# Kernel tuning notes

Measured on AMD Instinct MI355X. Metric: run time of the kernel, lower is better.

## Reference

```python
import jax, jax.numpy as jnp
import numpy as np

LENGTHSCALE = 0.3
EPS = 1e-10
N = 100000   # evaluation points
M = 3375     # grid_size**3 RBF centers


def setup_inputs() -> dict:
    key = jax.random.key(0)
    k1, k2, k3, k4, k5 = jax.random.split(key, 5)
    x = jax.random.normal(k1, (N, 3), dtype=jnp.float32)
    centers = jax.random.normal(k2, (M, 3), dtype=jnp.float32)
    coeff_u = jax.random.normal(k3, (M,), dtype=jnp.float32)
    coeff_v = jax.random.normal(k4, (M,), dtype=jnp.float32)
    coeff_w = jax.random.normal(k5, (M,), dtype=jnp.float32)
    return {"x": x, "centers": centers, "coeff_u": coeff_u,
            "coeff_v": coeff_v, "coeff_w": coeff_w}


def reference(x, centers, coeff_u, coeff_v, coeff_w):
    # base sphere-attractor field: x * (1 - ||x||)
    r = jnp.linalg.norm(x, axis=-1, keepdims=True)          # (N, 1)
    base = x * (1.0 - r)                                    # (N, 3)

    x_sq = jnp.sum(x * x, axis=-1, keepdims=True)           # (N, 1)
    c_sq = jnp.sum(centers * centers, axis=-1)[None, :]     # (1, M)
    xy = x @ centers.T                                      # (N, M)
    dist2 = jnp.maximum(x_sq + c_sq - 2.0 * xy, EPS)        # (N, M)

    # RBF features and three shared-phi matvecs fused as one matmul
    phi = jnp.exp(-dist2 / (2.0 * LENGTHSCALE ** 2))        # (N, M)
    coeffs = jnp.stack([coeff_u, coeff_v, coeff_w], axis=1) # (M, 3)
    uvw = phi @ coeffs                                      # (N, 3)
    return base + uvw
```

## Files before the change

kernel.cpp:

```cpp
#include <hip/hip_runtime.h>
#include <hip/hip_bf16.h>

#define S2 8.014973f
#define K2 16.029946f
#define CHUNKS 8

typedef float f2 __attribute__((ext_vector_type(2)));

__global__ void rbf_prep_kernel(const float* __restrict__ centers,
                                const float* __restrict__ cu,
                                const float* __restrict__ cv,
                                const float* __restrict__ cw,
                                float4* __restrict__ cpack, int M) {
    int m = blockIdx.x * 256 + threadIdx.x;
    if (m < M) {
        float cx = centers[3 * m + 0];
        float cy = centers[3 * m + 1];
        float cz = centers[3 * m + 2];
        float4 a, b;
        a.x = K2 * cx;
        a.y = K2 * cy;
        a.z = K2 * cz;
        a.w = -S2 * (cx * cx + cy * cy + cz * cz);
        b.x = cu[m];
        b.y = cv[m];
        b.z = cw[m];
        b.w = 0.f;
        cpack[2 * m + 0] = a;
        cpack[2 * m + 1] = b;
    }
}

__global__ __launch_bounds__(512) void rbf_main_kernel(
    const float* __restrict__ x, const float4* __restrict__ cpack,
    float* __restrict__ out, int N, int M) {
    __shared__ float acc[CHUNKS][128][3];

    const int tid = threadIdx.x;
    const int lane = tid & 63;
    const int chunk = __builtin_amdgcn_readfirstlane(tid >> 6);
    const int pbase = blockIdx.x * 128;
    const int p0 = pbase + lane;
    const int p1 = pbase + 64 + lane;

    float x00 = 0.f, x01 = 0.f, x02 = 0.f;
    float x10 = 0.f, x11 = 0.f, x12 = 0.f;
    if (p0 < N) {
        x00 = x[3 * p0 + 0];
        x01 = x[3 * p0 + 1];
        x02 = x[3 * p0 + 2];
    }
    if (p1 < N) {
        x10 = x[3 * p1 + 0];
        x11 = x[3 * p1 + 1];
        x12 = x[3 * p1 + 2];
    }

    const f2 X = {x00, x10};
    const f2 Y = {x01, x11};
    const f2 Z = {x02, x12};
    const f2 PX = {-S2 * (x00 * x00 + x01 * x01 + x02 * x02),
                   -S2 * (x10 * x10 + x11 * x11 + x12 * x12)};

    const int per = (M + CHUNKS - 1) / CHUNKS;
    const int jb = chunk * per;
    const int je = min(jb + per, M);

    f2 au = {0.f, 0.f}, av = {0.f, 0.f}, aw = {0.f, 0.f};

#pragma unroll 4
    for (int j = jb; j < je; ++j) {
        const float4 a = cpack[2 * j + 0];
        const float4 b = cpack[2 * j + 1];
        f2 e = PX + a.w;
        e += Z * a.z;
        e += Y * a.y;
        e += X * a.x;
        f2 phi;
        phi.x = __builtin_amdgcn_exp2f(e.x);
        phi.y = __builtin_amdgcn_exp2f(e.y);
        au += phi * b.x;
        av += phi * b.y;
        aw += phi * b.z;
    }

    if (chunk == 0) {
        float g0 = 1.f - sqrtf(x00 * x00 + x01 * x01 + x02 * x02);
        au.x += x00 * g0;
        av.x += x01 * g0;
        aw.x += x02 * g0;
        float g1 = 1.f - sqrtf(x10 * x10 + x11 * x11 + x12 * x12);
        au.y += x10 * g1;
        av.y += x11 * g1;
        aw.y += x12 * g1;
    }

    acc[chunk][lane][0] = au.x;
    acc[chunk][lane][1] = av.x;
    acc[chunk][lane][2] = aw.x;
    acc[chunk][64 + lane][0] = au.y;
    acc[chunk][64 + lane][1] = av.y;
    acc[chunk][64 + lane][2] = aw.y;
    __syncthreads();

    const int out_n = 3 * N;
    if (tid < 384) {
        int gi = pbase * 3 + tid;
        if (gi < out_n) {
            int pl = tid / 3;
            int c = tid % 3;
            float s = 0.f;
#pragma unroll
            for (int k = 0; k < CHUNKS; ++k) s += acc[k][pl][c];
            out[gi] = s;
        }
    }
}

extern "C" void kernel_launch(void* const* d_in, const int* in_sizes, int n_in,
                              void* d_out, int out_size, void* d_ws,
                              size_t ws_size, hipStream_t stream) {
    const float* x = (const float*)d_in[0];
    const float* centers = (const float*)d_in[1];
    const float* cu = (const float*)d_in[2];
    const float* cv = (const float*)d_in[3];
    const float* cw = (const float*)d_in[4];
    const int N = in_sizes[0] / 3;
    const int M = in_sizes[1] / 3;
    float4* cpack = (float4*)d_ws;
    float* out = (float*)d_out;

    hipLaunchKernelGGL(rbf_prep_kernel, dim3((M + 255) / 256), dim3(256), 0,
                       stream, centers, cu, cv, cw, cpack, M);
    hipLaunchKernelGGL(rbf_main_kernel, dim3((N + 127) / 128), dim3(512), 0,
                       stream, x, cpack, out, N, M);
}
```

Baseline: 139.4 us.

## Split center range across blocks and combine partial sums with atomic adds

The main kernel now divides the RBF centers into CSPLIT=4 groups spread over separate blocks, so the grid is four times larger. Each block reduces its eight waves in shared memory and atomically adds the partial result into an output that is zeroed first with hipMemsetAsync. The aim is better CU load balance and less tail imbalance from having only ~782 large blocks. In exchange, x is loaded redundantly, there is an extra memset, and the atomics make the floating-point summation order nondeterministic. The loop unroll also goes from 4 to 8, and the memset size assumes out_size is in bytes, which may not hold.

```diff
diff --git a/kernel.cpp b/kernel.cpp
--- a/kernel.cpp
+++ b/kernel.cpp
@@ -1,9 +1,9 @@
 #include <hip/hip_runtime.h>
-#include <hip/hip_bf16.h>
 
 #define S2 8.014973f
 #define K2 16.029946f
-#define CHUNKS 8
+#define WAVES 8
+#define CSPLIT 4
 
 typedef float f2 __attribute__((ext_vector_type(2)));
 
@@ -34,12 +34,13 @@
 __global__ __launch_bounds__(512) void rbf_main_kernel(
     const float* __restrict__ x, const float4* __restrict__ cpack,
     float* __restrict__ out, int N, int M) {
-    __shared__ float acc[CHUNKS][128][3];
+    __shared__ float acc[WAVES][128][3];
 
     const int tid = threadIdx.x;
     const int lane = tid & 63;
-    const int chunk = __builtin_amdgcn_readfirstlane(tid >> 6);
-    const int pbase = blockIdx.x * 128;
+    const int wave = __builtin_amdgcn_readfirstlane(tid >> 6);
+    const int cs = blockIdx.x & (CSPLIT - 1);
+    const int pbase = (blockIdx.x / CSPLIT) * 128;
     const int p0 = pbase + lane;
     const int p1 = pbase + 64 + lane;
 
@@ -62,13 +63,15 @@
     const f2 PX = {-S2 * (x00 * x00 + x01 * x01 + x02 * x02),
                    -S2 * (x10 * x10 + x11 * x11 + x12 * x12)};
 
-    const int per = (M + CHUNKS - 1) / CHUNKS;
-    const int jb = chunk * per;
-    const int je = min(jb + per, M);
+    const int g = cs * WAVES + wave;
+    const int per = (M + WAVES * CSPLIT - 1) / (WAVES * CSPLIT);
+    const int jb = g * per;
+    int je = jb + per;
+    if (je > M) je = M;
 
     f2 au = {0.f, 0.f}, av = {0.f, 0.f}, aw = {0.f, 0.f};
 
-#pragma unroll 4
+#pragma unroll 8
     for (int j = jb; j < je; ++j) {
         const float4 a = cpack[2 * j + 0];
         const float4 b = cpack[2 * j + 1];
@@ -84,7 +87,7 @@
         aw += phi * b.z;
     }
 
-    if (chunk == 0) {
+    if (g == 0) {
         float g0 = 1.f - sqrtf(x00 * x00 + x01 * x01 + x02 * x02);
         au.x += x00 * g0;
         av.x += x01 * g0;
@@ -95,24 +98,22 @@
         aw.y += x12 * g1;
     }
 
-    acc[chunk][lane][0] = au.x;
-    acc[chunk][lane][1] = av.x;
-    acc[chunk][lane][2] = aw.x;
-    acc[chunk][64 + lane][0] = au.y;
-    acc[chunk][64 + lane][1] = av.y;
-    acc[chunk][64 + lane][2] = aw.y;
+    acc[wave][lane][0] = au.x;
+    acc[wave][lane][1] = av.x;
+    acc[wave][lane][2] = aw.x;
+    acc[wave][64 + lane][0] = au.y;
+    acc[wave][64 + lane][1] = av.y;
+    acc[wave][64 + lane][2] = aw.y;
     __syncthreads();
 
-    const int out_n = 3 * N;
     if (tid < 384) {
-        int gi = pbase * 3 + tid;
-        if (gi < out_n) {
-            int pl = tid / 3;
-            int c = tid % 3;
+        const int gi = pbase * 3 + tid;
+        if (gi < 3 * N) {
+            const float* af = &acc[0][0][0];
             float s = 0.f;
 #pragma unroll
-            for (int k = 0; k < CHUNKS; ++k) s += acc[k][pl][c];
-            out[gi] = s;
+            for (int k = 0; k < WAVES; ++k) s += af[k * 384 + tid];
+            unsafeAtomicAdd(&out[gi], s);
         }
     }
 }
@@ -132,6 +133,8 @@
 
     hipLaunchKernelGGL(rbf_prep_kernel, dim3((M + 255) / 256), dim3(256), 0,
                        stream, centers, cu, cv, cw, cpack, M);
-    hipLaunchKernelGGL(rbf_main_kernel, dim3((N + 127) / 128), dim3(512), 0,
+    hipMemsetAsync(d_out, 0, (size_t)out_size, stream);
+    const int pt = (N + 127) / 128;
+    hipLaunchKernelGGL(rbf_main_kernel, dim3(pt * CSPLIT), dim3(512), 0,
                        stream, x, cpack, out, N, M);
 }
```

Measured after the change: 126.5 us. -9.3%, faster.

## Compute RBF exponents with bf16 MFMA using hi/lo split precision

Applied to the files above, without the earlier changes.

Replaces the scalar FMA computation of the RBF exponent with a 16x16x32 bf16 MFMA. Center and point coordinates are split into hi/lo bf16 pairs so that the dot products plus the squared-norm terms come out near fp32 accuracy. Each 64-thread block handles 16 points against all centers, and the per-lane partial sums are combined with cross-lane shuffles instead of a shared-memory reduction. The aim is to take the exponent arithmetic off the VALU and leave mainly exp2 and the coefficient FMAs there. The risks are precision loss from the bf16 splitting, since the dropped lo*lo terms are scaled by the large exponent factor, and many small single-wave blocks.

```diff
diff --git a/kernel.cpp b/kernel.cpp
--- a/kernel.cpp
+++ b/kernel.cpp
@@ -1,119 +1,128 @@
 #include <hip/hip_runtime.h>
-#include <hip/hip_bf16.h>
 
 #define S2 8.014973f
 #define K2 16.029946f
-#define CHUNKS 8
+#define ONEB ((unsigned short)0x3F80)
 
-typedef float f2 __attribute__((ext_vector_type(2)));
+typedef float f32x4 __attribute__((ext_vector_type(4)));
+typedef short bf16x8 __attribute__((ext_vector_type(8)));
 
-__global__ void rbf_prep_kernel(const float* __restrict__ centers,
-                                const float* __restrict__ cu,
-                                const float* __restrict__ cv,
-                                const float* __restrict__ cw,
-                                float4* __restrict__ cpack, int M) {
-    int m = blockIdx.x * 256 + threadIdx.x;
-    if (m < M) {
-        float cx = centers[3 * m + 0];
-        float cy = centers[3 * m + 1];
-        float cz = centers[3 * m + 2];
-        float4 a, b;
-        a.x = K2 * cx;
-        a.y = K2 * cy;
-        a.z = K2 * cz;
-        a.w = -S2 * (cx * cx + cy * cy + cz * cz);
-        b.x = cu[m];
-        b.y = cv[m];
-        b.z = cw[m];
-        b.w = 0.f;
-        cpack[2 * m + 0] = a;
-        cpack[2 * m + 1] = b;
+__device__ __forceinline__ unsigned short bhi(float v) {
+    unsigned int b = __builtin_bit_cast(unsigned int, v);
+    return (unsigned short)((b + 0x7FFFu + ((b >> 16) & 1u)) >> 16);
+}
+__device__ __forceinline__ float bf2f(unsigned short h) {
+    unsigned int u = ((unsigned int)h) << 16;
+    return __builtin_bit_cast(float, u);
+}
+
+__global__ void rbf_prep(const float* __restrict__ centers,
+                         const float* __restrict__ cu,
+                         const float* __restrict__ cv,
+                         const float* __restrict__ cw,
+                         uint4* __restrict__ afrag,
+                         float* __restrict__ bpack, int M) {
+    const int T = blockIdx.x;
+    const int lane = threadIdx.x;
+    const int row = lane & 15, g = lane >> 4;
+    const int c = T * 16 + row;
+    float cx = 0.f, cy = 0.f, cz = 0.f;
+    if (c < M) { cx = centers[3*c]; cy = centers[3*c+1]; cz = centers[3*c+2]; }
+    const float a1 = K2 * cx, a2 = K2 * cy, a3 = K2 * cz;
+    const float a4 = -S2 * (cx*cx + cy*cy + cz*cz);
+    const unsigned short a1h = bhi(a1), a2h = bhi(a2), a3h = bhi(a3), a4h = bhi(a4);
+    const unsigned short a1l = bhi(a1 - bf2f(a1h));
+    const unsigned short a2l = bhi(a2 - bf2f(a2h));
+    const unsigned short a3l = bhi(a3 - bf2f(a3h));
+    const unsigned short a4l = bhi(a4 - bf2f(a4h));
+    const unsigned short F[16] = {a1h, a1h, a1l, a2h, a2h, a2l, a3h, a3h,
+                                  a3l, a4h, a4l, ONEB, ONEB, 0, 0, 0};
+    uint4 u;
+    u.x = (unsigned int)F[8*g+0] | ((unsigned int)F[8*g+1] << 16);
+    u.y = (unsigned int)F[8*g+2] | ((unsigned int)F[8*g+3] << 16);
+    u.z = (unsigned int)F[8*g+4] | ((unsigned int)F[8*g+5] << 16);
+    u.w = (unsigned int)F[8*g+6] | ((unsigned int)F[8*g+7] << 16);
+    afrag[T * 64 + lane] = u;
+
+    if (lane < 48) {
+        const int g2 = lane / 12, idx = lane % 12;
+        const int comp = idx >> 2, r = idx & 3;
+        const int c2 = T * 16 + g2 * 4 + r;
+        float v = 0.f;
+        if (c2 < M)
+            v = (comp == 0) ? cu[c2] : ((comp == 1) ? cv[c2] : cw[c2]);
+        bpack[(T * 12 + g2 * 3 + comp) * 4 + r] = v;
     }
 }
 
-__global__ __launch_bounds__(512) void rbf_main_kernel(
-    const float* __restrict__ x, const float4* __restrict__ cpack,
-    float* __restrict__ out, int N, int M) {
-    __shared__ float acc[CHUNKS][128][3];
+__global__ __launch_bounds__(64) void rbf_main(
+        const float* __restrict__ x,
+        const uint4* __restrict__ afrag,
+        const float4* __restrict__ bpack4,
+        float* __restrict__ out, int N, int NT) {
+    const int lane = threadIdx.x;
+    const int col = lane & 15, g = lane >> 4;
+    const int p = blockIdx.x * 16 + col;
+    float xx = 0.f, xy = 0.f, xz = 0.f;
+    if (p < N) { xx = x[3*p]; xy = x[3*p+1]; xz = x[3*p+2]; }
+    const float px = -S2 * (xx*xx + xy*xy + xz*xz);
 
-    const int tid = threadIdx.x;
-    const int lane = tid & 63;
-    const int chunk = __builtin_amdgcn_readfirstlane(tid >> 6);
-    const int pbase = blockIdx.x * 128;
-    const int p0 = pbase + lane;
-    const int p1 = pbase + 64 + lane;
+    const unsigned short xh = bhi(xx), yh = bhi(xy), zh = bhi(xz);
+    const unsigned short xl = bhi(xx - bf2f(xh));
+    const unsigned short yl = bhi(xy - bf2f(yh));
+    const unsigned short zl = bhi(xz - bf2f(zh));
+    const unsigned short ph = bhi(px), pl = bhi(px - bf2f(ph));
+    unsigned int b0 = 0, b1 = 0, b2 = 0, b3 = 0;
+    if (g == 0) {
+        b0 = (unsigned int)xh | ((unsigned int)xl << 16);
+        b1 = (unsigned int)xh | ((unsigned int)yh << 16);
+        b2 = (unsigned int)yl | ((unsigned int)yh << 16);
+        b3 = (unsigned int)zh | ((unsigned int)zl << 16);
+    } else if (g == 1) {
+        b0 = (unsigned int)zh | ((unsigned int)ONEB << 16);
+        b1 = (unsigned int)ONEB | ((unsigned int)ph << 16);
+        b2 = (unsigned int)pl;
+        b3 = 0;
+    }
+    uint4 bu_;
+    bu_.x = b0; bu_.y = b1; bu_.z = b2; bu_.w = b3;
+    const bf16x8 bfrag = __builtin_bit_cast(bf16x8, bu_);
+    const f32x4 zero = {0.f, 0.f, 0.f, 0.f};
 
-    float x00 = 0.f, x01 = 0.f, x02 = 0.f;
-    float x10 = 0.f, x11 = 0.f, x12 = 0.f;
-    if (p0 < N) {
-        x00 = x[3 * p0 + 0];
-        x01 = x[3 * p0 + 1];
-        x02 = x[3 * p0 + 2];
-    }
-    if (p1 < N) {
-        x10 = x[3 * p1 + 0];
-        x11 = x[3 * p1 + 1];
-        x12 = x[3 * p1 + 2];
+    float au = 0.f, av = 0.f, aw = 0.f;
+    const uint4* __restrict__ ap = afrag + lane;
+    const float4* __restrict__ bp = bpack4 + g * 3;
+
+#pragma unroll 2
+    for (int T = 0; T < NT; ++T) {
+        const uint4 a = ap[T * 64];
+        const float4 bu = bp[T * 12 + 0];
+        const float4 bv = bp[T * 12 + 1];
+        const float4 bw = bp[T * 12 + 2];
+        const f32x4 E = __builtin_amdgcn_mfma_f32_16x16x32_bf16(
+            __builtin_bit_cast(bf16x8, a), bfrag, zero, 0, 0, 0);
+        const float p0 = __builtin_amdgcn_exp2f(E[0]);
+        const float p1 = __builtin_amdgcn_exp2f(E[1]);
+        const float p2 = __builtin_amdgcn_exp2f(E[2]);
+        const float p3 = __builtin_amdgcn_exp2f(E[3]);
+        au = fmaf(p0, bu.x, au); au = fmaf(p1, bu.y, au);
+        au = fmaf(p2, bu.z, au); au = fmaf(p3, bu.w, au);
+        av = fmaf(p0, bv.x, av); av = fmaf(p1, bv.y, av);
+        av = fmaf(p2, bv.z, av); av = fmaf(p3, bv.w, av);
+        aw = fmaf(p0, bw.x, aw); aw = fmaf(p1, bw.y, aw);
+        aw = fmaf(p2, bw.z, aw); aw = fmaf(p3, bw.w, aw);
     }
 
-    const f2 X = {x00, x10};
-    const f2 Y = {x01, x11};
-    const f2 Z = {x02, x12};
-    const f2 PX = {-S2 * (x00 * x00 + x01 * x01 + x02 * x02),
-                   -S2 * (x10 * x10 + x11 * x11 + x12 * x12)};
+    au += __shfl_xor(au, 16); au += __shfl_xor(au, 32);
+    av += __shfl_xor(av, 16); av += __shfl_xor(av, 32);
+    aw += __shfl_xor(aw, 16); aw += __shfl_xor(aw, 32);
 
-    const int per = (M + CHUNKS - 1) / CHUNKS;
-    const int jb = chunk * per;
-    const int je = min(jb + per, M);
-
-    f2 au = {0.f, 0.f}, av = {0.f, 0.f}, aw = {0.f, 0.f};
-
-#pragma unroll 4
-    for (int j = jb; j < je; ++j) {
-        const float4 a = cpack[2 * j + 0];
-        const float4 b = cpack[2 * j + 1];
-        f2 e = PX + a.w;
-        e += Z * a.z;
-        e += Y * a.y;
-        e += X * a.x;
-        f2 phi;
-        phi.x = __builtin_amdgcn_exp2f(e.x);
-        phi.y = __builtin_amdgcn_exp2f(e.y);
-        au += phi * b.x;
-        av += phi * b.y;
-        aw += phi * b.z;
-    }
-
-    if (chunk == 0) {
-        float g0 = 1.f - sqrtf(x00 * x00 + x01 * x01 + x02 * x02);
-        au.x += x00 * g0;
-        av.x += x01 * g0;
-        aw.x += x02 * g0;
-        float g1 = 1.f - sqrtf(x10 * x10 + x11 * x11 + x12 * x12);
-        au.y += x10 * g1;
-        av.y += x11 * g1;
-        aw.y += x12 * g1;
-    }
-
-    acc[chunk][lane][0] = au.x;
-    acc[chunk][lane][1] = av.x;
-    acc[chunk][lane][2] = aw.x;
-    acc[chunk][64 + lane][0] = au.y;
-    acc[chunk][64 + lane][1] = av.y;
-    acc[chunk][64 + lane][2] = aw.y;
-    __syncthreads();
-
-    const int out_n = 3 * N;
-    if (tid < 384) {
-        int gi = pbase * 3 + tid;
-        if (gi < out_n) {
-            int pl = tid / 3;
-            int c = tid % 3;
-            float s = 0.f;
-#pragma unroll
-            for (int k = 0; k < CHUNKS; ++k) s += acc[k][pl][c];
-            out[gi] = s;
-        }
+    if (g == 0 && p < N) {
+        const float r = sqrtf(xx*xx + xy*xy + xz*xz);
+        const float s = 1.f - r;
+        out[3*p+0] = fmaf(xx, s, au);
+        out[3*p+1] = fmaf(xy, s, av);
+        out[3*p+2] = fmaf(xz, s, aw);
     }
 }
 
@@ -125,13 +134,16 @@
     const float* cu = (const float*)d_in[2];
     const float* cv = (const float*)d_in[3];
     const float* cw = (const float*)d_in[4];
+    float* out = (float*)d_out;
     const int N = in_sizes[0] / 3;
     const int M = in_sizes[1] / 3;
-    float4* cpack = (float4*)d_ws;
-    float* out = (float*)d_out;
+    const int NT = (M + 15) / 16;
 
-    hipLaunchKernelGGL(rbf_prep_kernel, dim3((M + 255) / 256), dim3(256), 0,
-                       stream, centers, cu, cv, cw, cpack, M);
-    hipLaunchKernelGGL(rbf_main_kernel, dim3((N + 127) / 128), dim3(512), 0,
-                       stream, x, cpack, out, N, M);
+    uint4* afrag = (uint4*)d_ws;
+    float* bpack = (float*)((char*)d_ws + (size_t)NT * 1024);
+
+    hipLaunchKernelGGL(rbf_prep, dim3(NT), dim3(64), 0, stream,
+                       centers, cu, cv, cw, afrag, bpack, M);
+    hipLaunchKernelGGL(rbf_main, dim3((N + 15) / 16), dim3(64), 0, stream,
+                       x, afrag, (const float4*)bpack, out, N, NT);
 }
```

Result: slower. 220.5 us (+58.2%).
